# Optimization experiments

Hardware: AMD Instinct MI355X
Metric: run time of the kernel (lower is better)

## Reference

```python
import jax, jax.numpy as jnp
import numpy as np

H, L, N = 128, 8192, 64


def setup_inputs() -> dict:
    key = jax.random.key(0)
    ks = jax.random.split(key, 8)
    u = jax.random.normal(ks[0], (H, L), jnp.float32)
    # lecun_normal-scaled params, per channel
    Ct_ri = jax.random.normal(ks[1], (H, N, 2), jnp.float32) / np.sqrt(N)
    B_raw = jax.random.normal(ks[2], (H, N, 1), jnp.float32) / np.sqrt(N)
    D = jax.random.uniform(ks[3], (H,), jnp.float32)
    lo, hi = np.log(0.001), np.log(0.1)
    log_step = jax.random.uniform(ks[4], (H,), jnp.float32) * (hi - lo) + lo
    n = np.arange(N, dtype=np.float32)
    Lambda_re = jnp.full((N,), -0.5, jnp.float32)
    Lambda_im = jnp.asarray(np.pi * n, jnp.float32)
    p_re = jnp.asarray(np.sqrt(n + 0.5), jnp.float32)
    p_im = jnp.zeros((N,), jnp.float32)
    q_re = jnp.asarray(np.sqrt(n + 0.5), jnp.float32)
    q_im = jnp.zeros((N,), jnp.float32)
    Vc_re = jax.random.normal(ks[5], (N, N), jnp.float32) / np.sqrt(N)
    Vc_im = jax.random.normal(ks[6], (N, N), jnp.float32) / np.sqrt(N)
    return dict(u=u, Ct_ri=Ct_ri, B_raw=B_raw, D=D, log_step=log_step,
                Lambda_re=Lambda_re, Lambda_im=Lambda_im,
                p_re=p_re, p_im=p_im, q_re=q_re, q_im=q_im,
                Vc_re=Vc_re, Vc_im=Vc_im)


def _s4_forward(u, Ct_ri, B_raw, D, log_step,
                Lambda_re, Lambda_im, p_re, p_im, q_re, q_im, Vc_re, Vc_im):
    h, l = u.shape
    Lambda = (Lambda_re + 1j * Lambda_im).astype(jnp.complex64)   # (N,)
    p = (p_re + 1j * p_im).astype(jnp.complex64)                  # (N,)
    q = (q_re + 1j * q_im).astype(jnp.complex64)                  # (N,)
    Vc = (Vc_re + 1j * Vc_im).astype(jnp.complex64)               # (N,N)
    Ct = (Ct_ri[..., 0] + 1j * Ct_ri[..., 1]).astype(jnp.complex64)  # (H,N)
    # B = Vc @ B_raw  per channel -> (H,N)
    B = jnp.einsum('nm,hm->hn', Vc, B_raw[..., 0].astype(jnp.complex64))
    step = jnp.exp(log_step)                                      # (H,)

    # K_gen_DPLR evaluated at the L roots of unity (conv_from_gen)
    omega = jnp.exp(-2j * jnp.pi * (jnp.arange(l) / l)).astype(jnp.complex64)  # (L,)
    g = (2.0 / step)[:, None] * ((1.0 - omega) / (1.0 + omega))[None, :]       # (H,L)
    c = 2.0 / (1.0 + omega)                                                    # (L,)

    # cauchy_dot: sum_n a_n / (g - Lambda_n); reuse one (H,L,N) reciprocal
    recip = 1.0 / (g[:, :, None] - Lambda[None, None, :])          # (H,L,N)
    Ctc = Ct.conj()
    k00 = jnp.einsum('hn,hln->hl', Ctc * B, recip)
    k01 = jnp.einsum('hn,hln->hl', Ctc * p[None, :], recip)
    k10 = jnp.einsum('hn,hln->hl', q.conj()[None, :] * B, recip)
    k11 = jnp.einsum('n,hln->hl', q.conj() * p, recip)
    at_roots = c[None, :] * (k00 - k01 * (1.0 / (1.0 + k11)) * k10)  # (H,L)

    K = jnp.fft.ifft(at_roots, n=l, axis=-1).real                 # (H,L)

    # non_circular_convolution via zero-padded rfft
    ud = jnp.fft.rfft(jnp.pad(u, ((0, 0), (0, l))), axis=-1)
    Kd = jnp.fft.rfft(jnp.pad(K, ((0, 0), (0, l))), axis=-1)
    y = jnp.fft.irfft(ud * Kd, axis=-1)[:, :l]                    # (H,L)
    return y + D[:, None] * u


def reference(u, Ct_ri, B_raw, D, log_step,
              Lambda_re, Lambda_im, p_re, p_im, q_re, q_im, Vc_re, Vc_im):
    return _s4_forward(u, Ct_ri, B_raw, D, log_step,
                       Lambda_re, Lambda_im, p_re, p_im, q_re, q_im,
                       Vc_re, Vc_im)
```

## Files before the change

kernel.cpp:

```cpp
#include <hip/hip_runtime.h>
#include <math.h>

#define H 128
#define L 8192
#define NSTATE 64
#define NTH 1024
#define PI_D 3.14159265358979323846
#define RT2 0.70710678118654752440f

#define W16K_RE 0.99999992646571789f
#define W16K_IM (-3.8349518757139556e-4f)
#define W32K_RE 0.99999998161642898f
#define W32K_IM (-1.9174759731070332e-4f)

typedef float v2f __attribute__((ext_vector_type(2)));

__device__ __forceinline__ v2f pkfma(v2f a, v2f b, v2f c) {
    return __builtin_elementwise_fma(a, b, c);
}
__device__ __forceinline__ v2f pkfma(float a, v2f b, v2f c) {
    v2f av = a; return __builtin_elementwise_fma(av, b, c);
}

__device__ __forceinline__ int SWZ(int e) { return e ^ ((e >> 3) & 7); }
__device__ __forceinline__ int TSW(int j) { return j ^ ((j >> 4) & 15) ^ ((j >> 8) & 15); }
__device__ __forceinline__ int brev13(int x) { return (int)(__brev((unsigned)x) >> 19); }

__device__ __forceinline__ float2 cmul(float2 a, float2 b) {
    return make_float2(a.x * b.x - a.y * b.y, a.x * b.y + a.y * b.x);
}
__device__ __forceinline__ float2 cmulc(float2 w, float2 x) {
    return make_float2(w.x * x.x + w.y * x.y, w.x * x.y - w.y * x.x);
}
__device__ __forceinline__ float2 cadd(float2 a, float2 b) { return make_float2(a.x + b.x, a.y + b.y); }
__device__ __forceinline__ float2 csub(float2 a, float2 b) { return make_float2(a.x - b.x, a.y - b.y); }
__device__ __forceinline__ float2 mnegi(float2 a) { return make_float2(a.y, -a.x); }
__device__ __forceinline__ float2 mposi(float2 a) { return make_float2(-a.y, a.x); }

template<bool INV>
__device__ __forceinline__ float2 twget(const float2* __restrict__ tw, int idx) {
    float2 w;
    if (idx < 2048) w = tw[TSW(idx)];
    else { float2 t = tw[TSW(idx - 2048)]; w = make_float2(t.y, -t.x); }
    if (INV) w.y = -w.y;
    return w;
}

template<int SIGMA>
__device__ __forceinline__ void dif_pass1(float2* __restrict__ A,
                                          const float2* __restrict__ tw, int tid) {
    const int m1 = 2048 / SIGMA;
    #pragma unroll
    for (int rep = 0; rep < 2; ++rep) {
        int q = tid + rep * NTH;
        int r = q & (SIGMA - 1);
        int b = ((q & ~(SIGMA - 1)) << 2) | r;
        float2 w1 = tw[TSW(r * m1)];
        float2 w2 = cmul(w1, w1);
        float2 w1b = mnegi(w1);
        int i0 = SWZ(b), i1 = SWZ(b + SIGMA), i2 = SWZ(b + 2 * SIGMA), i3 = SWZ(b + 3 * SIGMA);
        float2 x0 = A[i0], x1 = A[i1], x2 = A[i2], x3 = A[i3];
        float2 y0 = cadd(x0, x2), y2 = cmul(csub(x0, x2), w1);
        float2 y1 = cadd(x1, x3), y3 = cmul(csub(x1, x3), w1b);
        A[i0] = cadd(y0, y1); A[i1] = cmul(csub(y0, y1), w2);
        A[i2] = cadd(y2, y3); A[i3] = cmul(csub(y2, y3), w2);
    }
}

template<int SIGMA>
__device__ __forceinline__ void dit_pass1(float2* __restrict__ A,
                                          const float2* __restrict__ tw, int tid) {
    const int m1 = 2048 / SIGMA;
    #pragma unroll
    for (int rep = 0; rep < 2; ++rep) {
        int q = tid + rep * NTH;
        int r = q & (SIGMA - 1);
        int b = ((q & ~(SIGMA - 1)) << 2) | r;
        float2 v1 = tw[TSW(r * m1)];
        float2 v2 = cmul(v1, v1);
        int i0 = SWZ(b), i1 = SWZ(b + SIGMA), i2 = SWZ(b + 2 * SIGMA), i3 = SWZ(b + 3 * SIGMA);
        float2 x0 = A[i0], x1 = A[i1], x2 = A[i2], x3 = A[i3];
        float2 t1 = cmulc(v2, x1);
        float2 y0 = cadd(x0, t1), y1 = csub(x0, t1);
        float2 t3 = cmulc(v2, x3);
        float2 y2 = cadd(x2, t3), y3 = csub(x2, t3);
        float2 u2 = cmulc(v1, y2);
        A[i0] = cadd(y0, u2); A[i2] = csub(y0, u2);
        float2 u3 = mposi(cmulc(v1, y3));
        A[i1] = cadd(y1, u3); A[i3] = csub(y1, u3);
    }
}

template<int P>
__device__ __forceinline__ void cauchy_chunk(
    const int type, const int tid, const float two_over_step,
    const float2* __restrict__ tw,
    const float4* __restrict__ wq, const float2* __restrict__ wr,
    const float4* __restrict__ wp,
    float* __restrict__ specRe, float* __restrict__ specIm)
{
    const float2 W16K = make_float2(W16K_RE, W16K_IM);
    const float2 W32K = make_float2(W32K_RE, W32K_IM);
    float tk0, tk1;
    v2f gv;
    #pragma unroll
    for (int e = 0; e < 2; ++e) {
        int k = brev13(8 * tid + 2 * P + e);
        float2 w;
        if (e == 0) {
            w = tw[TSW(k >> 1)];
        } else {
            float2 t0 = tw[TSW((k >> 1) - 2048)];
            w = make_float2(t0.y, -t0.x);
        }
        if (k & 1) w = cmul(w, W16K);
        if (type)  w = cmul(w, W32K);
        float t = -w.y * __builtin_amdgcn_rcpf(w.x);
        t = fminf(fmaxf(t, -3.0e7f), 3.0e7f);
        if (e == 0) { tk0 = t; gv.x = two_over_step * t; }
        else        { tk1 = t; gv.y = two_over_step * t; }
    }
    v2f A00x = 0.f, A00y = 0.f, A01x = 0.f, A01y = 0.f;
    v2f A10x = 0.f, A10y = 0.f, A11x = 0.f, A11y = 0.f;
    #pragma unroll 2
    for (int n = 0; n < NSTATE; ++n) {
        float4 qv = wq[n];
        float2 rv = wr[n];
        float4 pv = wp[n];
        v2f dim = gv - pv.z;
        v2f dre2 = pv.y;
        v2f den = pkfma(dim, dim, dre2);
        v2f inv; inv.x = __builtin_amdgcn_rcpf(den.x);
                 inv.y = __builtin_amdgcn_rcpf(den.y);
        v2f rre = pv.x * inv;
        v2f rim = -(dim * inv);
        A00x = pkfma(qv.x, rre, pkfma(-qv.y, rim, A00x));
        A00y = pkfma(qv.x, rim, pkfma( qv.y, rre, A00y));
        A01x = pkfma(qv.z, rre, pkfma(-qv.w, rim, A01x));
        A01y = pkfma(qv.z, rim, pkfma( qv.w, rre, A01y));
        A10x = pkfma(rv.x, rre, pkfma(-rv.y, rim, A10x));
        A10y = pkfma(rv.x, rim, pkfma( rv.y, rre, A10y));
        A11x = pkfma(pv.w, rre, A11x);
        A11y = pkfma(pv.w, rim, A11y);
    }
    #pragma unroll
    for (int e = 0; e < 2; ++e) {
        float2 a00 = make_float2(e ? A00x.y : A00x.x, e ? A00y.y : A00y.x);
        float2 a01 = make_float2(e ? A01x.y : A01x.x, e ? A01y.y : A01y.x);
        float2 a10 = make_float2(e ? A10x.y : A10x.x, e ? A10y.y : A10y.x);
        float2 a11 = make_float2(e ? A11x.y : A11x.x, e ? A11y.y : A11y.x);
        float tt = e ? tk1 : tk0;
        float2 den1 = make_float2(1.0f + a11.x, a11.y);
        float invd = 1.0f / (den1.x * den1.x + den1.y * den1.y);
        float2 qn = cmul(a01, a10);
        float2 dv = make_float2((qn.x * den1.x + qn.y * den1.y) * invd,
                                (qn.y * den1.x - qn.x * den1.y) * invd);
        float2 tmp = make_float2(a00.x - dv.x, a00.y - dv.y);
        float2 s = cmul(make_float2(1.0f, tt), tmp);
        int j = 2 * P + e;
        specRe[j * NTH + tid] = s.x;
        specIm[j * NTH + tid] = s.y;
    }
}

__global__ __launch_bounds__(NSTATE)
void s4_prep(const float* __restrict__ Ct_ri, const float* __restrict__ B_raw,
             const float* __restrict__ Lre_g, const float* __restrict__ Lim_g,
             const float* __restrict__ p_re, const float* __restrict__ p_im,
             const float* __restrict__ q_re, const float* __restrict__ q_im,
             const float* __restrict__ Vc_re, const float* __restrict__ Vc_im,
             char* __restrict__ ws)
{
    const int h = blockIdx.x, n = threadIdx.x;
    float2 Bc = make_float2(0.f, 0.f);
    for (int m = 0; m < NSTATE; ++m) {
        float br = B_raw[h * NSTATE + m];
        Bc.x += Vc_re[n * NSTATE + m] * br;
        Bc.y += Vc_im[n * NSTATE + m] * br;
    }
    float2 Ctc = make_float2(Ct_ri[(h * NSTATE + n) * 2 + 0],
                             -Ct_ri[(h * NSTATE + n) * 2 + 1]);
    float2 pc = make_float2(p_re[n], p_im[n]);
    float2 qc = make_float2(q_re[n], -q_im[n]);
    float2 w00 = cmul(Ctc, Bc);
    float2 w01 = cmul(Ctc, pc);
    float2 w10 = cmul(qc, Bc);
    float2 w11 = cmul(qc, pc);
    float dre = -Lre_g[n];
    float4* wq = (float4*)ws;
    float2* wr = (float2*)(ws + (size_t)H * NSTATE * 16);
    float4* wp = (float4*)(ws + (size_t)H * NSTATE * 24);
    wq[h * NSTATE + n] = make_float4(w00.x, w00.y, w01.x, w01.y);
    wr[h * NSTATE + n] = make_float2(w10.x, w10.y);
    wp[h * NSTATE + n] = make_float4(dre, dre * dre, Lim_g[n], w11.x);
}

__global__ __launch_bounds__(256)
void s4_combine(float4* __restrict__ out, const float4* __restrict__ yneg) {
    int i = blockIdx.x * 256 + threadIdx.x;
    float4 a = out[i], b = yneg[i];
    out[i] = make_float4(a.x + b.x, a.y + b.y, a.z + b.z, a.w + b.w);
}

extern __shared__ char smem_raw[];

template<bool WG, bool SP>
__global__ __launch_bounds__(NTH)
void s4_split_kernel(const float* __restrict__ u,
                     const float* __restrict__ Ct_ri,
                     const float* __restrict__ B_raw,
                     const float* __restrict__ Dp,
                     const float* __restrict__ log_step,
                     const float* __restrict__ Lre_g,
                     const float* __restrict__ Lim_g,
                     const float* __restrict__ p_re,
                     const float* __restrict__ p_im,
                     const float* __restrict__ q_re,
                     const float* __restrict__ q_im,
                     const float* __restrict__ Vc_re,
                     const float* __restrict__ Vc_im,
                     const char* __restrict__ wsw,
                     float* __restrict__ yneg,
                     float* __restrict__ out)
{
    float2* bufA   = (float2*)smem_raw;
    float2* tw     = bufA + L;
    float*  specRe = (float*)(tw + 2048);
    float*  specIm = specRe + L;
    float4* wq4    = (float4*)(specIm + L);
    float2* wr2    = (float2*)(wq4 + NSTATE);
    float4* wp4    = (float4*)(wr2 + NSTATE);

    const int bid  = blockIdx.x;
    const int type = bid >> 7;
    const int h    = bid & (H - 1);
    const int tid  = threadIdx.x;

    for (int j = tid; j < 2048; j += NTH) {
        double a = -2.0 * PI_D * (double)j / (double)L;
        tw[TSW(j)] = make_float2((float)cos(a), (float)sin(a));
    }
    const float4* wqp; const float2* wrp; const float4* wpp;
    if constexpr (WG) {
        wqp = (const float4*)wsw + (size_t)h * NSTATE;
        wrp = (const float2*)(wsw + (size_t)H * NSTATE * 16) + (size_t)h * NSTATE;
        wpp = (const float4*)(wsw + (size_t)H * NSTATE * 24) + (size_t)h * NSTATE;
    } else {
        if (tid < NSTATE) {
            int n = tid;
            float2 Bc = make_float2(0.f, 0.f);
            for (int m = 0; m < NSTATE; ++m) {
                float br = B_raw[h * NSTATE + m];
                Bc.x += Vc_re[n * NSTATE + m] * br;
                Bc.y += Vc_im[n * NSTATE + m] * br;
            }
            float2 Ctc = make_float2(Ct_ri[(h * NSTATE + n) * 2 + 0],
                                     -Ct_ri[(h * NSTATE + n) * 2 + 1]);
            float2 pc = make_float2(p_re[n], p_im[n]);
            float2 qc = make_float2(q_re[n], -q_im[n]);
            float2 w00 = cmul(Ctc, Bc);
            float2 w01 = cmul(Ctc, pc);
            float2 w10 = cmul(qc, Bc);
            float2 w11 = cmul(qc, pc);
            float dre = -Lre_g[n];
            wq4[n] = make_float4(w00.x, w00.y, w01.x, w01.y);
            wr2[n] = make_float2(w10.x, w10.y);
            wp4[n] = make_float4(dre, dre * dre, Lim_g[n], w11.x);
        }
        wqp = wq4; wrp = wr2; wpp = wp4;
    }
    if constexpr (!WG) __syncthreads();

    const float step = expf(log_step[h]);
    const float two_over_step = 2.0f / step;
    const float Dh = Dp[h];
    const float* ur = u + (size_t)h * L;
    const float2 W16K = make_float2(W16K_RE, W16K_IM);

    for (int i = tid; i < L; i += NTH) {
        float uv = ur[i];
        if (type == 0) {
            bufA[SWZ(i)] = make_float2(uv, 0.f);
        } else {
            float2 w = twget<false>(tw, i >> 1);
            if (i & 1) w = cmul(w, W16K);
            bufA[SWZ(i)] = make_float2(uv * w.x, uv * w.y);
        }
    }
    cauchy_chunk<0>(type, tid, two_over_step, tw, wqp, wrp, wpp, specRe, specIm);
    __syncthreads();

    dif_pass1<2048>(bufA, tw, tid);
    cauchy_chunk<1>(type, tid, two_over_step, tw, wqp, wrp, wpp, specRe, specIm);
    __syncthreads();
    dif_pass1<512>(bufA, tw, tid);
    cauchy_chunk<2>(type, tid, two_over_step, tw, wqp, wrp, wpp, specRe, specIm);
    __syncthreads();
    dif_pass1<128>(bufA, tw, tid);
    cauchy_chunk<3>(type, tid, two_over_step, tw, wqp, wrp, wpp, specRe, specIm);
    __syncthreads();
    dif_pass1<32>(bufA, tw, tid);   __syncthreads();
    dif_pass1<8>(bufA, tw, tid);    __syncthreads();

    {
        const int base = tid * 8;
        float2 x0 = bufA[SWZ(base + 0)], x1 = bufA[SWZ(base + 1)];
        float2 x2 = bufA[SWZ(base + 2)], x3 = bufA[SWZ(base + 3)];
        float2 x4 = bufA[SWZ(base + 4)], x5 = bufA[SWZ(base + 5)];
        float2 x6 = bufA[SWZ(base + 6)], x7 = bufA[SWZ(base + 7)];
        float2 a0 = cadd(x0, x4), a1 = cadd(x1, x5), a2 = cadd(x2, x6), a3 = cadd(x3, x7);
        float2 s0 = csub(x0, x4), s1 = csub(x1, x5), s2 = csub(x2, x6), s3 = csub(x3, x7);
        float2 b0 = s0;
        float2 b1 = cmul(s1, make_float2(RT2, -RT2));
        float2 b2 = mnegi(s2);
        float2 b3 = cmul(s3, make_float2(-RT2, -RT2));
        float2 c0 = cadd(a0, a2), c2 = csub(a0, a2);
        float2 c1 = cadd(a1, a3), c3 = mnegi(csub(a1, a3));
        float2 d0 = cadd(b0, b2), d2 = csub(b0, b2);
        float2 d1 = cadd(b1, b3), d3 = mnegi(csub(b1, b3));
        float2 y0 = cadd(c0, c1), y1 = csub(c0, c1);
        float2 y2 = cadd(c2, c3), y3 = csub(c2, c3);
        float2 y4 = cadd(d0, d1), y5 = csub(d0, d1);
        float2 y6 = cadd(d2, d3), y7 = csub(d2, d3);
        y0 = cmul(y0, make_float2(specRe[0 * NTH + tid], specIm[0 * NTH + tid]));
        y1 = cmul(y1, make_float2(specRe[1 * NTH + tid], specIm[1 * NTH + tid]));
        y2 = cmul(y2, make_float2(specRe[2 * NTH + tid], specIm[2 * NTH + tid]));
        y3 = cmul(y3, make_float2(specRe[3 * NTH + tid], specIm[3 * NTH + tid]));
        y4 = cmul(y4, make_float2(specRe[4 * NTH + tid], specIm[4 * NTH + tid]));
        y5 = cmul(y5, make_float2(specRe[5 * NTH + tid], specIm[5 * NTH + tid]));
        y6 = cmul(y6, make_float2(specRe[6 * NTH + tid], specIm[6 * NTH + tid]));
        y7 = cmul(y7, make_float2(specRe[7 * NTH + tid], specIm[7 * NTH + tid]));
        float2 e0 = cadd(y0, y1), e1 = csub(y0, y1), e2 = cadd(y2, y3), e3 = csub(y2, y3);
        float2 e4 = cadd(y4, y5), e5 = csub(y4, y5), e6 = cadd(y6, y7), e7 = csub(y6, y7);
        float2 f0 = cadd(e0, e2), f2 = csub(e0, e2);
        float2 ti = mposi(e3); float2 f1 = cadd(e1, ti), f3 = csub(e1, ti);
        float2 f4 = cadd(e4, e6), f6 = csub(e4, e6);
        float2 tj = mposi(e7); float2 f5 = cadd(e5, tj), f7 = csub(e5, tj);
        float2 g4 = f4;
        float2 g5 = cmul(make_float2(RT2, RT2), f5);
        float2 g6 = mposi(f6);
        float2 g7 = cmul(make_float2(-RT2, RT2), f7);
        bufA[SWZ(base + 0)] = cadd(f0, g4); bufA[SWZ(base + 4)] = csub(f0, g4);
        bufA[SWZ(base + 1)] = cadd(f1, g5); bufA[SWZ(base + 5)] = csub(f1, g5);
        bufA[SWZ(base + 2)] = cadd(f2, g6); bufA[SWZ(base + 6)] = csub(f2, g6);
        bufA[SWZ(base + 3)] = cadd(f3, g7); bufA[SWZ(base + 7)] = csub(f3, g7);
    }
    __syncthreads();

    dit_pass1<8>(bufA, tw, tid);    __syncthreads();
    dit_pass1<32>(bufA, tw, tid);   __syncthreads();
    dit_pass1<128>(bufA, tw, tid);  __syncthreads();
    dit_pass1<512>(bufA, tw, tid);  __syncthreads();
    dit_pass1<2048>(bufA, tw, tid); __syncthreads();

    const float sc = 0.5f / (float)L;
    float* orow = out + (size_t)h * L;
    float* yrow = SP ? (yneg + (size_t)h * L) : nullptr;
    for (int t = tid; t < L; t += NTH) {
        float2 z = bufA[SWZ(t)];
        float val;
        if (type == 0) {
            val = z.x * sc + Dh * ur[t];
        } else {
            float2 w = twget<false>(tw, t >> 1);
            if (t & 1) w = cmul(w, W16K);
            val = (w.x * z.x + w.y * z.y) * sc;
        }
        if constexpr (SP) {
            if (type == 0) orow[t] = val; else yrow[t] = val;
        } else {
            atomicAdd(&orow[t], val);
        }
    }
}

extern "C" void kernel_launch(void* const* d_in, const int* in_sizes, int n_in,
                              void* d_out, int out_size, void* d_ws, size_t ws_size,
                              hipStream_t stream) {
    (void)in_sizes; (void)n_in; (void)out_size;
    const float* u        = (const float*)d_in[0];
    const float* Ct_ri    = (const float*)d_in[1];
    const float* B_raw    = (const float*)d_in[2];
    const float* Dp       = (const float*)d_in[3];
    const float* log_step = (const float*)d_in[4];
    const float* Lre      = (const float*)d_in[5];
    const float* Lim      = (const float*)d_in[6];
    const float* p_re     = (const float*)d_in[7];
    const float* p_im     = (const float*)d_in[8];
    const float* q_re     = (const float*)d_in[9];
    const float* q_im     = (const float*)d_in[10];
    const float* Vc_re    = (const float*)d_in[11];
    const float* Vc_im    = (const float*)d_in[12];
    float* out = (float*)d_out;

    const size_t needW = (size_t)H * NSTATE * (16 + 8 + 16);
    const size_t needY = needW + (size_t)H * L * sizeof(float);
    const bool wg = ws_size >= needW;
    const bool sp = ws_size >= needY;

    char*  wsw  = (char*)d_ws;
    float* yneg = (float*)((char*)d_ws + needW);

    const size_t smemW = (size_t)(L + 2048) * sizeof(float2)
                       + (size_t)2 * L * sizeof(float);
    const size_t smemL = smemW + NSTATE * (16 + 8 + 16);

    if (wg) {
        s4_prep<<<dim3(H), dim3(NSTATE), 0, stream>>>(
            Ct_ri, B_raw, Lre, Lim, p_re, p_im, q_re, q_im, Vc_re, Vc_im, wsw);
        if (sp) {
            hipFuncSetAttribute((const void*)s4_split_kernel<true, true>,
                                hipFuncAttributeMaxDynamicSharedMemorySize, (int)smemW);
            s4_split_kernel<true, true><<<dim3(2 * H), dim3(NTH), smemW, stream>>>(
                u, Ct_ri, B_raw, Dp, log_step, Lre, Lim,
                p_re, p_im, q_re, q_im, Vc_re, Vc_im, wsw, yneg, out);
            s4_combine<<<dim3((H * L) / (256 * 4)), dim3(256), 0, stream>>>(
                (float4*)out, (const float4*)yneg);
        } else {
            hipMemsetAsync(out, 0, (size_t)H * L * sizeof(float), stream);
            hipFuncSetAttribute((const void*)s4_split_kernel<true, false>,
                                hipFuncAttributeMaxDynamicSharedMemorySize, (int)smemW);
            s4_split_kernel<true, false><<<dim3(2 * H), dim3(NTH), smemW, stream>>>(
                u, Ct_ri, B_raw, Dp, log_step, Lre, Lim,
                p_re, p_im, q_re, q_im, Vc_re, Vc_im, wsw, nullptr, out);
        }
    } else {
        hipMemsetAsync(out, 0, (size_t)H * L * sizeof(float), stream);
        hipFuncSetAttribute((const void*)s4_split_kernel<false, false>,
                            hipFuncAttributeMaxDynamicSharedMemorySize, (int)smemL);
        s4_split_kernel<false, false><<<dim3(2 * H), dim3(NTH), smemL, stream>>>(
            u, Ct_ri, B_raw, Dp, log_step, Lre, Lim,
            p_re, p_im, q_re, q_im, Vc_re, Vc_im, nullptr, nullptr, out);
    }
}
```

Baseline: 80.45 us.

## Fuse input load into first FFT pass, output store into last, share reciprocals

The global load and twiddle premultiply of u are folded into the first radix-4 DIF pass, and the last DIT pass is folded into the scaled output store. This removes two LDS round trips and two block barriers. The Cauchy inner loop also computes both reciprocals from one rcp of the product, with the imaginary-sign handling moved into the accumulate coefficients. In exchange, the shared reciprocal may lose accuracy or overflow when both denominators are large, and the WG path now takes an unconditional barrier.

```diff
diff --git a/kernel.cpp b/kernel.cpp
--- a/kernel.cpp
+++ b/kernel.cpp
@@ -36,15 +36,6 @@
 __device__ __forceinline__ float2 csub(float2 a, float2 b) { return make_float2(a.x - b.x, a.y - b.y); }
 __device__ __forceinline__ float2 mnegi(float2 a) { return make_float2(a.y, -a.x); }
 __device__ __forceinline__ float2 mposi(float2 a) { return make_float2(-a.y, a.x); }
-
-template<bool INV>
-__device__ __forceinline__ float2 twget(const float2* __restrict__ tw, int idx) {
-    float2 w;
-    if (idx < 2048) w = tw[TSW(idx)];
-    else { float2 t = tw[TSW(idx - 2048)]; w = make_float2(t.y, -t.x); }
-    if (INV) w.y = -w.y;
-    return w;
-}
 
 template<int SIGMA>
 __device__ __forceinline__ void dif_pass1(float2* __restrict__ A,
@@ -91,6 +82,93 @@
     }
 }
 
+__device__ __forceinline__ void dif_first_load(float2* __restrict__ A,
+                                               const float2* __restrict__ tw,
+                                               int tid, const float* __restrict__ ur,
+                                               int type) {
+    #pragma unroll
+    for (int rep = 0; rep < 2; ++rep) {
+        int q = tid + rep * NTH;
+        float u0 = ur[q], u1 = ur[q + 2048], u2v = ur[q + 4096], u3v = ur[q + 6144];
+        float2 x0, x1, x2, x3;
+        if (type == 0) {
+            x0 = make_float2(u0, 0.f); x1 = make_float2(u1, 0.f);
+            x2 = make_float2(u2v, 0.f); x3 = make_float2(u3v, 0.f);
+        } else {
+            int hq = q >> 1;
+            float2 wa = tw[TSW(hq)];
+            float2 wb = tw[TSW(hq + 1024)];
+            float2 adj = (q & 1) ? make_float2(W16K_RE, W16K_IM) : make_float2(1.f, 0.f);
+            wa = cmul(wa, adj); wb = cmul(wb, adj);
+            float2 wc = mnegi(wa), wd = mnegi(wb);
+            x0 = make_float2(u0 * wa.x, u0 * wa.y);
+            x1 = make_float2(u1 * wb.x, u1 * wb.y);
+            x2 = make_float2(u2v * wc.x, u2v * wc.y);
+            x3 = make_float2(u3v * wd.x, u3v * wd.y);
+        }
+        float2 w1 = tw[TSW(q)];
+        float2 w2 = cmul(w1, w1);
+        float2 w1b = mnegi(w1);
+        float2 y0 = cadd(x0, x2), y2 = cmul(csub(x0, x2), w1);
+        float2 y1 = cadd(x1, x3), y3 = cmul(csub(x1, x3), w1b);
+        A[SWZ(q)]        = cadd(y0, y1);
+        A[SWZ(q + 2048)] = cmul(csub(y0, y1), w2);
+        A[SWZ(q + 4096)] = cadd(y2, y3);
+        A[SWZ(q + 6144)] = cmul(csub(y2, y3), w2);
+    }
+}
+
+template<bool SP>
+__device__ __forceinline__ void dit_last_store(const float2* __restrict__ A,
+                                               const float2* __restrict__ tw,
+                                               int tid, int type,
+                                               const float* __restrict__ ur, float Dh,
+                                               float* __restrict__ orow,
+                                               float* __restrict__ yrow) {
+    const float sc = 0.5f / (float)L;
+    #pragma unroll
+    for (int rep = 0; rep < 2; ++rep) {
+        int q = tid + rep * NTH;
+        float2 v1 = tw[TSW(q)];
+        float2 v2 = cmul(v1, v1);
+        float2 x0 = A[SWZ(q)], x1 = A[SWZ(q + 2048)];
+        float2 x2 = A[SWZ(q + 4096)], x3 = A[SWZ(q + 6144)];
+        float2 t1 = cmulc(v2, x1);
+        float2 y0 = cadd(x0, t1), y1 = csub(x0, t1);
+        float2 t3 = cmulc(v2, x3);
+        float2 y2 = cadd(x2, t3), y3 = csub(x2, t3);
+        float2 u2c = cmulc(v1, y2);
+        float2 z0 = cadd(y0, u2c), z2 = csub(y0, u2c);
+        float2 u3c = mposi(cmulc(v1, y3));
+        float2 z1 = cadd(y1, u3c), z3 = csub(y1, u3c);
+        float v0, vv1, vv2, vv3;
+        if (type == 0) {
+            v0  = z0.x * sc + Dh * ur[q];
+            vv1 = z1.x * sc + Dh * ur[q + 2048];
+            vv2 = z2.x * sc + Dh * ur[q + 4096];
+            vv3 = z3.x * sc + Dh * ur[q + 6144];
+        } else {
+            int hq = q >> 1;
+            float2 wa = tw[TSW(hq)];
+            float2 wb = tw[TSW(hq + 1024)];
+            float2 adj = (q & 1) ? make_float2(W16K_RE, W16K_IM) : make_float2(1.f, 0.f);
+            wa = cmul(wa, adj); wb = cmul(wb, adj);
+            float2 wc = mnegi(wa), wd = mnegi(wb);
+            v0  = (wa.x * z0.x + wa.y * z0.y) * sc;
+            vv1 = (wb.x * z1.x + wb.y * z1.y) * sc;
+            vv2 = (wc.x * z2.x + wc.y * z2.y) * sc;
+            vv3 = (wd.x * z3.x + wd.y * z3.y) * sc;
+        }
+        float* dst = (type == 0) ? orow : (SP ? yrow : orow);
+        if constexpr (SP) {
+            dst[q] = v0; dst[q + 2048] = vv1; dst[q + 4096] = vv2; dst[q + 6144] = vv3;
+        } else {
+            atomicAdd(&dst[q], v0); atomicAdd(&dst[q + 2048], vv1);
+            atomicAdd(&dst[q + 4096], vv2); atomicAdd(&dst[q + 6144], vv3);
+        }
+    }
+}
+
 template<int P>
 __device__ __forceinline__ void cauchy_chunk(
     const int type, const int tid, const float two_over_step,
@@ -130,18 +208,18 @@
         v2f dim = gv - pv.z;
         v2f dre2 = pv.y;
         v2f den = pkfma(dim, dim, dre2);
-        v2f inv; inv.x = __builtin_amdgcn_rcpf(den.x);
-                 inv.y = __builtin_amdgcn_rcpf(den.y);
+        float rp = __builtin_amdgcn_rcpf(den.x * den.y);
+        v2f inv; inv.x = den.y * rp; inv.y = den.x * rp;
         v2f rre = pv.x * inv;
-        v2f rim = -(dim * inv);
-        A00x = pkfma(qv.x, rre, pkfma(-qv.y, rim, A00x));
-        A00y = pkfma(qv.x, rim, pkfma( qv.y, rre, A00y));
-        A01x = pkfma(qv.z, rre, pkfma(-qv.w, rim, A01x));
-        A01y = pkfma(qv.z, rim, pkfma( qv.w, rre, A01y));
-        A10x = pkfma(rv.x, rre, pkfma(-rv.y, rim, A10x));
-        A10y = pkfma(rv.x, rim, pkfma( rv.y, rre, A10y));
-        A11x = pkfma(pv.w, rre, A11x);
-        A11y = pkfma(pv.w, rim, A11y);
+        v2f rip = dim * inv;
+        A00x = pkfma(qv.x, rre, pkfma( qv.y, rip, A00x));
+        A00y = pkfma(qv.y, rre, pkfma(-qv.x, rip, A00y));
+        A01x = pkfma(qv.z, rre, pkfma( qv.w, rip, A01x));
+        A01y = pkfma(qv.w, rre, pkfma(-qv.z, rip, A01y));
+        A10x = pkfma(rv.x, rre, pkfma( rv.y, rip, A10x));
+        A10y = pkfma(rv.y, rre, pkfma(-rv.x, rip, A10y));
+        A11x = pkfma( pv.w, rre, A11x);
+        A11y = pkfma(-pv.w, rip, A11y);
     }
     #pragma unroll
     for (int e = 0; e < 2; ++e) {
@@ -269,37 +347,25 @@
         }
         wqp = wq4; wrp = wr2; wpp = wp4;
     }
-    if constexpr (!WG) __syncthreads();
+    __syncthreads();
 
     const float step = expf(log_step[h]);
     const float two_over_step = 2.0f / step;
     const float Dh = Dp[h];
     const float* ur = u + (size_t)h * L;
-    const float2 W16K = make_float2(W16K_RE, W16K_IM);
-
-    for (int i = tid; i < L; i += NTH) {
-        float uv = ur[i];
-        if (type == 0) {
-            bufA[SWZ(i)] = make_float2(uv, 0.f);
-        } else {
-            float2 w = twget<false>(tw, i >> 1);
-            if (i & 1) w = cmul(w, W16K);
-            bufA[SWZ(i)] = make_float2(uv * w.x, uv * w.y);
-        }
-    }
+
+    dif_first_load(bufA, tw, tid, ur, type);
     cauchy_chunk<0>(type, tid, two_over_step, tw, wqp, wrp, wpp, specRe, specIm);
     __syncthreads();
-
-    dif_pass1<2048>(bufA, tw, tid);
+    dif_pass1<512>(bufA, tw, tid);
     cauchy_chunk<1>(type, tid, two_over_step, tw, wqp, wrp, wpp, specRe, specIm);
     __syncthreads();
-    dif_pass1<512>(bufA, tw, tid);
+    dif_pass1<128>(bufA, tw, tid);
     cauchy_chunk<2>(type, tid, two_over_step, tw, wqp, wrp, wpp, specRe, specIm);
     __syncthreads();
-    dif_pass1<128>(bufA, tw, tid);
+    dif_pass1<32>(bufA, tw, tid);
     cauchy_chunk<3>(type, tid, two_over_step, tw, wqp, wrp, wpp, specRe, specIm);
     __syncthreads();
-    dif_pass1<32>(bufA, tw, tid);   __syncthreads();
     dif_pass1<8>(bufA, tw, tid);    __syncthreads();
 
     {
@@ -351,27 +417,9 @@
     dit_pass1<32>(bufA, tw, tid);   __syncthreads();
     dit_pass1<128>(bufA, tw, tid);  __syncthreads();
     dit_pass1<512>(bufA, tw, tid);  __syncthreads();
-    dit_pass1<2048>(bufA, tw, tid); __syncthreads();
-
-    const float sc = 0.5f / (float)L;
-    float* orow = out + (size_t)h * L;
-    float* yrow = SP ? (yneg + (size_t)h * L) : nullptr;
-    for (int t = tid; t < L; t += NTH) {
-        float2 z = bufA[SWZ(t)];
-        float val;
-        if (type == 0) {
-            val = z.x * sc + Dh * ur[t];
-        } else {
-            float2 w = twget<false>(tw, t >> 1);
-            if (t & 1) w = cmul(w, W16K);
-            val = (w.x * z.x + w.y * z.y) * sc;
-        }
-        if constexpr (SP) {
-            if (type == 0) orow[t] = val; else yrow[t] = val;
-        } else {
-            atomicAdd(&orow[t], val);
-        }
-    }
+    dit_last_store<SP>(bufA, tw, tid, type, ur, Dh,
+                       out + (size_t)h * L,
+                       SP ? (yneg + (size_t)h * L) : nullptr);
 }
 
 extern "C" void kernel_launch(void* const* d_in, const int* in_sizes, int n_in,
```

Result: no change. 79.58 us (-1.1%).
